# Performance work log

Hardware: AMD Instinct MI355X
Metric: run time of the kernel (lower is better)

Reference implementation:

```python
import jax, jax.numpy as jnp
import numpy as np

NUM_SCALES = 3
LAMBDA_0 = 1.0
MU_0 = 1.0
KAPPA_LAMBDA = 0.5
KAPPA_MU = 0.5
BASE_WEIGHT = 1.0
GRADIENT_SCALING = 0.1


def tgradient(f, axis):
    """torch.gradient semantics: central diff interior, one-sided at edges (spacing=1)."""
    n = f.shape[axis]
    def sl(a, b):
        idx = [slice(None)] * f.ndim
        idx[axis] = slice(a, b)
        return f[tuple(idx)]
    interior = (sl(2, n) - sl(0, n - 2)) * 0.5
    first = sl(1, 2) - sl(0, 1)
    last = sl(n - 1, n) - sl(n - 2, n - 1)
    return jnp.concatenate([first, interior, last], axis=axis)


def resize1d_linear(x, axis, out_size):
    """1D linear resize along `axis` with align_corners=True."""
    in_size = x.shape[axis]
    if out_size == in_size:
        return x
    denom = max(out_size - 1, 1)
    coords = jnp.arange(out_size, dtype=jnp.float32) * ((in_size - 1) / denom)
    i0 = jnp.floor(coords).astype(jnp.int32)
    i1 = jnp.minimum(i0 + 1, in_size - 1)
    w = (coords - i0.astype(jnp.float32)).astype(x.dtype)
    shape = [1] * x.ndim
    shape[axis] = out_size
    w = w.reshape(shape)
    x0 = jnp.take(x, i0, axis=axis)
    x1 = jnp.take(x, i1, axis=axis)
    return x0 * (1 - w) + x1 * w


def trilinear_downsample(x, scale):
    # F.interpolate(..., scale_factor=1/scale, mode='trilinear', align_corners=True,
    # recompute_scale_factor=True): out_size = floor(in_size / scale); separable linear.
    for axis in (2, 3, 4):
        out_size = int(np.floor(x.shape[axis] / scale))
        x = resize1d_linear(x, axis, out_size)
    return x


def elasticity_loss(deformation_field, image):
    total_loss = jnp.float32(0.0)
    for i in range(NUM_SCALES):
        scale = 2 ** i
        deform = trilinear_downsample(deformation_field, scale)
        img = trilinear_downsample(image, scale)
        u, v, w = deform[:, 0], deform[:, 1], deform[:, 2]  # each (B, X, Y, Z)
        du_dx, du_dy, du_dz = tgradient(u, 1), tgradient(u, 2), tgradient(u, 3)
        dv_dx, dv_dy, dv_dz = tgradient(v, 1), tgradient(v, 2), tgradient(v, 3)
        dw_dx, dw_dy, dw_dz = tgradient(w, 1), tgradient(w, 2), tgradient(w, 3)
        E_xx, E_yy, E_zz = du_dx, dv_dy, dw_dz
        E_xy = 0.5 * (du_dy + dv_dx)
        E_xz = 0.5 * (du_dz + dw_dx)
        E_yz = 0.5 * (dv_dz + dw_dy)
        trace_E = E_xx + E_yy + E_zz
        ic = img[:, 0]  # (B, X, Y, Z)
        gx, gy, gz = tgradient(ic, 1), tgradient(ic, 2), tgradient(ic, 3)
        image_gradient = jnp.sqrt(gx * gx + gy * gy + gz * gz)
        adaptive_lambda = LAMBDA_0 + KAPPA_LAMBDA * image_gradient
        adaptive_mu = MU_0 + KAPPA_MU * image_gradient
        elastic_energy = (0.5 * adaptive_lambda * trace_E ** 2
                          + adaptive_mu * (E_xx ** 2 + E_yy ** 2 + E_zz ** 2
                                           + 2.0 * (E_xy ** 2 + E_xz ** 2 + E_yz ** 2)))
        adaptive_weight = BASE_WEIGHT + GRADIENT_SCALING * image_gradient
        total_loss = total_loss + jnp.mean(adaptive_weight * elastic_energy)
    return total_loss


def setup_inputs() -> dict:
    key = jax.random.key(0)
    k1, k2 = jax.random.split(key)
    deformation_field = jax.random.normal(k1, (2, 3, 160, 192, 160), dtype=jnp.float32)
    image = jax.random.uniform(k2, (2, 1, 160, 192, 160), dtype=jnp.float32)
    return {"deformation_field": deformation_field, "image": image}


def reference(deformation_field, image):
    return elasticity_loss(deformation_field, image)
```

## Files before the change

### kernel.cpp

```cpp
#include <hip/hip_runtime.h>
#include <math.h>


#define LAMBDA_0 1.0f
#define MU_0 1.0f
#define KAPPA_LAMBDA 0.5f
#define KAPPA_MU 0.5f
#define BASE_WEIGHT 1.0f
#define GRADIENT_SCALING 0.1f

constexpr int TY = 32;
constexpr int TZ = 32;
constexpr int CX = 10;
constexpr int PITCH = TZ + 4;
constexpr int ROWS = TY + 2;
constexpr int FSZ = ROWS * PITCH;

struct P4 {
    float4 a, b, c, d;
    float ha, hb, hc, hd;
};

__device__ __forceinline__ P4 loadPlane(const float* __restrict__ p0,
                                        const float* __restrict__ p1,
                                        const float* __restrict__ p2,
                                        const float* __restrict__ p3,
                                        long long po, long long ctrOff,
                                        bool hasHalo, long long haloOff) {
    P4 r;
    long long o = po + ctrOff;
    r.a = *(const float4*)(p0 + o);
    r.b = *(const float4*)(p1 + o);
    r.c = *(const float4*)(p2 + o);
    r.d = *(const float4*)(p3 + o);
    r.ha = r.hb = r.hc = r.hd = 0.f;
    if (hasHalo) {
        long long h = po + haloOff;
        r.ha = p0[h]; r.hb = p1[h]; r.hc = p2[h]; r.hd = p3[h];
    }
    return r;
}

__device__ __forceinline__ void storePlane(float* lds, const P4& pr,
                                           int ldsCtr, bool hasHalo, int hIdx) {
    *(float4*)(lds + 0 * FSZ + ldsCtr) = pr.a;
    *(float4*)(lds + 1 * FSZ + ldsCtr) = pr.b;
    *(float4*)(lds + 2 * FSZ + ldsCtr) = pr.c;
    *(float4*)(lds + 3 * FSZ + ldsCtr) = pr.d;
    if (hasHalo) {
        lds[0 * FSZ + hIdx] = pr.ha;
        lds[1 * FSZ + hIdx] = pr.hb;
        lds[2 * FSZ + hIdx] = pr.hc;
        lds[3 * FSZ + hIdx] = pr.hd;
    }
}

__device__ __forceinline__ void unpackC(const P4& p, float d[4][4]) {
    d[0][0] = p.a.x; d[0][1] = p.a.y; d[0][2] = p.a.z; d[0][3] = p.a.w;
    d[1][0] = p.b.x; d[1][1] = p.b.y; d[1][2] = p.b.z; d[1][3] = p.b.w;
    d[2][0] = p.c.x; d[2][1] = p.c.y; d[2][2] = p.c.z; d[2][3] = p.c.w;
    d[3][0] = p.d.x; d[3][1] = p.d.y; d[3][2] = p.d.z; d[3][3] = p.d.w;
}

__global__ void elasticity_stream_kernel(const float* __restrict__ def,
                                         const float* __restrict__ img,
                                         int X, int Y, int Z,
                                         int nby, int nbz, int nbx,
                                         float inv_n, float* __restrict__ out) {
    __shared__ __align__(16) float lds[4 * FSZ];

    int t = blockIdx.x;
    const int bx = t % nbx; t /= nbx;
    const int bz = t % nbz; t /= nbz;
    const int by = t % nby; t /= nby;
    const int b = t;

    const int tz = bz * TZ, ty = by * TY, x0 = bx * CX;
    const int tid = threadIdx.x;
    const int zg = tid & 7;
    const int ly = tid >> 3;

    const long long vol = (long long)X * Y * Z;
    const long long sX = (long long)Y * Z;
    const float* __restrict__ p0 = def + ((long long)b * 3 + 0) * vol;
    const float* __restrict__ p1 = def + ((long long)b * 3 + 1) * vol;
    const float* __restrict__ p2 = def + ((long long)b * 3 + 2) * vol;
    const float* __restrict__ p3 = img + (long long)b * vol;

    const int gy = ty + ly;
    const int gz0 = tz + 4 * zg;
    const long long ctrOff = (long long)gy * Z + gz0;
    const int ldsCtr = (ly + 1) * PITCH + 4 * zg;

    const bool hasHalo = (tid < 2 * (TZ + 2) + 2 * TY);
    int hIdx = 0;
    long long haloOff = 0;
    if (hasHalo) {
        int hr, hc;
        if (tid < TZ + 2)                { hr = 0;      hc = tid; }
        else if (tid < 2 * (TZ + 2))     { hr = TY + 1; hc = tid - (TZ + 2); }
        else if (tid < 2 * (TZ + 2) + TY){ hr = tid - 2 * (TZ + 2) + 1; hc = TZ; }
        else                             { hr = tid - (2 * (TZ + 2) + TY) + 1; hc = TZ + 1; }
        int zl = (hc < TZ) ? hc : ((hc == TZ) ? -1 : TZ);
        int hy = min(max(ty + hr - 1, 0), Y - 1);
        int hz = min(max(tz + zl, 0), Z - 1);
        haloOff = (long long)hy * Z + hz;
        hIdx = hr * PITCH + hc;
    }

    const bool ylo = (gy == 0), yhi = (gy == Y - 1);
    const bool zloE = (gz0 == 0), zhiE = (gz0 + 4 == Z);
    const int zmCol = (zg == 0) ? TZ : (4 * zg - 1);
    const int zpCol = (zg == 7) ? (TZ + 1) : (4 * zg + 4);
    const int rowM = ly * PITCH + 4 * zg;
    const int rowC = (ly + 1) * PITCH;
    const int rowP = (ly + 2) * PITCH + 4 * zg;

    float Cprev[4][4], Ccur[4][4], Cnext[4][4];
    {
        long long o = (long long)max(x0 - 1, 0) * sX + ctrOff;
        float4 a = *(const float4*)(p0 + o);
        float4 bq = *(const float4*)(p1 + o);
        float4 c = *(const float4*)(p2 + o);
        float4 d = *(const float4*)(p3 + o);
        Cprev[0][0]=a.x; Cprev[0][1]=a.y; Cprev[0][2]=a.z; Cprev[0][3]=a.w;
        Cprev[1][0]=bq.x;Cprev[1][1]=bq.y;Cprev[1][2]=bq.z;Cprev[1][3]=bq.w;
        Cprev[2][0]=c.x; Cprev[2][1]=c.y; Cprev[2][2]=c.z; Cprev[2][3]=c.w;
        Cprev[3][0]=d.x; Cprev[3][1]=d.y; Cprev[3][2]=d.z; Cprev[3][3]=d.w;
    }
    P4 cur = loadPlane(p0, p1, p2, p3, (long long)x0 * sX, ctrOff, hasHalo, haloOff);
    storePlane(lds, cur, ldsCtr, hasHalo, hIdx);
    unpackC(cur, Ccur);
    __syncthreads();
    P4 pn = loadPlane(p0, p1, p2, p3, (long long)(x0 + 1) * sX, ctrOff, hasHalo, haloOff);

    float acc = 0.f;
    for (int i = 0; i < CX; ++i) {
        const int x = x0 + i;
        const bool xlo = (x == 0), xhi = (x == X - 1);

        P4 q;
        const bool more = (i + 1 < CX);
        if (more) {
            long long xp = min(x + 2, X - 1);
            q = loadPlane(p0, p1, p2, p3, xp * sX, ctrOff, hasHalo, haloOff);
        }

        unpackC(pn, Cnext);

        float GX[4][4], GY[4][4], GZ[4][4];
#pragma unroll
        for (int f = 0; f < 4; ++f) {
            const float* L = lds + f * FSZ;
            float4 ym = *(const float4*)(L + rowM);
            float4 yp = *(const float4*)(L + rowP);
            float zm = L[rowC + zmCol];
            float zp = L[rowC + zpCol];
            float ymv[4] = {ym.x, ym.y, ym.z, ym.w};
            float ypv[4] = {yp.x, yp.y, yp.z, yp.w};
#pragma unroll
            for (int i2 = 0; i2 < 4; ++i2) {
                float C = Ccur[f][i2];
                GX[f][i2] = xlo ? (Cnext[f][i2] - C)
                                : (xhi ? (C - Cprev[f][i2])
                                       : 0.5f * (Cnext[f][i2] - Cprev[f][i2]));
                GY[f][i2] = ylo ? (ypv[i2] - C)
                                : (yhi ? (C - ymv[i2])
                                       : 0.5f * (ypv[i2] - ymv[i2]));
            }
            GZ[f][0] = zloE ? (Ccur[f][1] - Ccur[f][0]) : 0.5f * (Ccur[f][1] - zm);
            GZ[f][1] = 0.5f * (Ccur[f][2] - Ccur[f][0]);
            GZ[f][2] = 0.5f * (Ccur[f][3] - Ccur[f][1]);
            GZ[f][3] = zhiE ? (Ccur[f][3] - Ccur[f][2]) : 0.5f * (zp - Ccur[f][2]);
        }

#pragma unroll
        for (int i2 = 0; i2 < 4; ++i2) {
            float Exx = GX[0][i2], Eyy = GY[1][i2], Ezz = GZ[2][i2];
            float Exy = 0.5f * (GY[0][i2] + GX[1][i2]);
            float Exz = 0.5f * (GZ[0][i2] + GX[2][i2]);
            float Eyz = 0.5f * (GZ[1][i2] + GY[2][i2]);
            float tr = Exx + Eyy + Ezz;
            float g = sqrtf(GX[3][i2] * GX[3][i2] + GY[3][i2] * GY[3][i2] +
                            GZ[3][i2] * GZ[3][i2]);
            float lam = LAMBDA_0 + KAPPA_LAMBDA * g;
            float mu  = MU_0 + KAPPA_MU * g;
            float energy = 0.5f * lam * tr * tr +
                           mu * (Exx * Exx + Eyy * Eyy + Ezz * Ezz +
                                 2.0f * (Exy * Exy + Exz * Exz + Eyz * Eyz));
            float wgt = BASE_WEIGHT + GRADIENT_SCALING * g;
            acc += wgt * energy;
        }

        if (more) {
            __syncthreads();
            storePlane(lds, pn, ldsCtr, hasHalo, hIdx);
            __syncthreads();
#pragma unroll
            for (int f = 0; f < 4; ++f)
#pragma unroll
                for (int i2 = 0; i2 < 4; ++i2) {
                    Cprev[f][i2] = Ccur[f][i2];
                    Ccur[f][i2] = Cnext[f][i2];
                }
            pn = q;
        }
    }

    float val = acc * inv_n;
    for (int off = 32; off > 0; off >>= 1)
        val += __shfl_down(val, off, 64);
    __shared__ float smem[4];
    int lane = threadIdx.x & 63;
    int wid = (int)(threadIdx.x >> 6);
    if (lane == 0) smem[wid] = val;
    __syncthreads();
    if (threadIdx.x == 0) {
        float s = smem[0] + smem[1] + smem[2] + smem[3];
        atomicAdd(out, s);
    }
}


__global__ void downsample3d_kernel(const float* __restrict__ in,
                                    float* __restrict__ out,
                                    int nmaps,
                                    int inX, int inY, int inZ,
                                    int outX, int outY, int outZ,
                                    float rx, float ry, float rz) {
    long long total = (long long)nmaps * outX * outY * outZ;
    long long idx = (long long)blockIdx.x * blockDim.x + threadIdx.x;
    if (idx >= total) return;

    int z = (int)(idx % outZ);
    long long t = idx / outZ;
    int y = (int)(t % outY);
    t /= outY;
    int x = (int)(t % outX);
    int m = (int)(t / outX);

    float cx = (float)x * rx;
    float cy = (float)y * ry;
    float cz = (float)z * rz;
    int ix0 = (int)floorf(cx), iy0 = (int)floorf(cy), iz0 = (int)floorf(cz);
    float wx = cx - (float)ix0, wy = cy - (float)iy0, wz = cz - (float)iz0;
    int ix1 = min(ix0 + 1, inX - 1);
    int iy1 = min(iy0 + 1, inY - 1);
    int iz1 = min(iz0 + 1, inZ - 1);

    long long sYZ = (long long)inY * inZ;
    const float* p = in + (long long)m * inX * sYZ;

    long long bx0 = (long long)ix0 * sYZ, bx1 = (long long)ix1 * sYZ;
    long long by0 = (long long)iy0 * inZ, by1 = (long long)iy1 * inZ;

    float v000 = p[bx0 + by0 + iz0], v001 = p[bx0 + by0 + iz1];
    float v010 = p[bx0 + by1 + iz0], v011 = p[bx0 + by1 + iz1];
    float v100 = p[bx1 + by0 + iz0], v101 = p[bx1 + by0 + iz1];
    float v110 = p[bx1 + by1 + iz0], v111 = p[bx1 + by1 + iz1];

    float a00 = v000 * (1.f - wx) + v100 * wx;
    float a01 = v001 * (1.f - wx) + v101 * wx;
    float a10 = v010 * (1.f - wx) + v110 * wx;
    float a11 = v011 * (1.f - wx) + v111 * wx;
    float b0 = a00 * (1.f - wy) + a10 * wy;
    float b1 = a01 * (1.f - wy) + a11 * wy;
    out[idx] = b0 * (1.f - wz) + b1 * wz;
}

__global__ void elasticity_loss_v4_kernel(const float* __restrict__ def,
                                          const float* __restrict__ img,
                                          int B, int X, int Y, int Z,
                                          float inv_n,
                                          float* __restrict__ out) {
    const int Zg = Z >> 2;
    long long total = (long long)B * X * Y * Zg;
    long long idx = (long long)blockIdx.x * blockDim.x + threadIdx.x;
    float val = 0.f;
    if (idx < total) {
        int zg = (int)(idx % Zg);
        long long t = idx / Zg;
        int y = (int)(t % Y);
        t /= Y;
        int x = (int)(t % X);
        int b = (int)(t / X);
        int z0 = zg << 2;

        long long vol = (long long)X * Y * Z;
        const float* base0 = def + ((long long)b * 3 + 0) * vol;
        const float* base1 = def + ((long long)b * 3 + 1) * vol;
        const float* base2 = def + ((long long)b * 3 + 2) * vol;
        const float* base3 = img + (long long)b * vol;
        const float* bases[4] = {base0, base1, base2, base3};

        long long sX = (long long)Y * Z;
        long long c = (long long)x * sX + (long long)y * Z + z0;
        long long cxm = (x > 0) ? c - sX : c;
        long long cxp = (x < X - 1) ? c + sX : c;
        long long cym = (y > 0) ? c - Z : c;
        long long cyp = (y < Y - 1) ? c + Z : c;
        long long czm = (z0 > 0) ? c - 1 : c;
        long long czp = (z0 + 4 < Z) ? c + 4 : c;

        float C[4][4], XM[4][4], XP[4][4], YM[4][4], YP[4][4];
        float ZM[4], ZP[4];
#pragma unroll
        for (int f = 0; f < 4; ++f) {
            const float* p = bases[f];
            float4 tc = *(const float4*)(p + c);
            float4 txm = *(const float4*)(p + cxm);
            float4 txp = *(const float4*)(p + cxp);
            float4 tym = *(const float4*)(p + cym);
            float4 typ = *(const float4*)(p + cyp);
            ZM[f] = p[czm];
            ZP[f] = p[czp];
            C[f][0] = tc.x;  C[f][1] = tc.y;  C[f][2] = tc.z;  C[f][3] = tc.w;
            XM[f][0] = txm.x; XM[f][1] = txm.y; XM[f][2] = txm.z; XM[f][3] = txm.w;
            XP[f][0] = txp.x; XP[f][1] = txp.y; XP[f][2] = txp.z; XP[f][3] = txp.w;
            YM[f][0] = tym.x; YM[f][1] = tym.y; YM[f][2] = tym.z; YM[f][3] = tym.w;
            YP[f][0] = typ.x; YP[f][1] = typ.y; YP[f][2] = typ.z; YP[f][3] = typ.w;
        }

        const bool xlo = (x == 0), xhi = (x == X - 1);
        const bool ylo = (y == 0), yhi = (y == Y - 1);
        const bool zlo = (z0 == 0), zhi = (z0 + 4 == Z);

        float GX[4][4], GY[4][4], GZ[4][4];
#pragma unroll
        for (int f = 0; f < 4; ++f) {
#pragma unroll
            for (int i = 0; i < 4; ++i) {
                GX[f][i] = xlo ? (XP[f][i] - C[f][i])
                               : (xhi ? (C[f][i] - XM[f][i])
                                      : 0.5f * (XP[f][i] - XM[f][i]));
                GY[f][i] = ylo ? (YP[f][i] - C[f][i])
                               : (yhi ? (C[f][i] - YM[f][i])
                                      : 0.5f * (YP[f][i] - YM[f][i]));
            }
            GZ[f][0] = zlo ? (C[f][1] - C[f][0]) : 0.5f * (C[f][1] - ZM[f]);
            GZ[f][1] = 0.5f * (C[f][2] - C[f][0]);
            GZ[f][2] = 0.5f * (C[f][3] - C[f][1]);
            GZ[f][3] = zhi ? (C[f][3] - C[f][2]) : 0.5f * (ZP[f] - C[f][2]);
        }

        float acc = 0.f;
#pragma unroll
        for (int i = 0; i < 4; ++i) {
            float Exx = GX[0][i], Eyy = GY[1][i], Ezz = GZ[2][i];
            float Exy = 0.5f * (GY[0][i] + GX[1][i]);
            float Exz = 0.5f * (GZ[0][i] + GX[2][i]);
            float Eyz = 0.5f * (GZ[1][i] + GY[2][i]);
            float tr = Exx + Eyy + Ezz;
            float g = sqrtf(GX[3][i] * GX[3][i] + GY[3][i] * GY[3][i] +
                            GZ[3][i] * GZ[3][i]);
            float lam = LAMBDA_0 + KAPPA_LAMBDA * g;
            float mu  = MU_0 + KAPPA_MU * g;
            float energy = 0.5f * lam * tr * tr +
                           mu * (Exx * Exx + Eyy * Eyy + Ezz * Ezz +
                                 2.0f * (Exy * Exy + Exz * Exz + Eyz * Eyz));
            float wgt = BASE_WEIGHT + GRADIENT_SCALING * g;
            acc += wgt * energy;
        }
        val = acc * inv_n;
    }

    for (int off = 32; off > 0; off >>= 1)
        val += __shfl_down(val, off, 64);
    __shared__ float smem[8];
    int lane = threadIdx.x & 63;
    int wid = (int)(threadIdx.x >> 6);
    if (lane == 0) smem[wid] = val;
    __syncthreads();
    if (threadIdx.x == 0) {
        float s = 0.f;
        int nw = (int)(blockDim.x >> 6);
        for (int i = 0; i < nw; ++i) s += smem[i];
        atomicAdd(out, s);
    }
}

static void launch_loss_v4(const float* def, const float* img, int B, int X,
                           int Y, int Z, float* out, hipStream_t stream) {
    const int BLOCK = 256;
    long long nvox = (long long)B * X * Y * Z;
    long long total = nvox >> 2;
    float inv_n = (float)(1.0 / (double)nvox);
    int grid = (int)((total + BLOCK - 1) / BLOCK);
    elasticity_loss_v4_kernel<<<grid, BLOCK, 0, stream>>>(def, img, B, X, Y, Z,
                                                          inv_n, out);
}

extern "C" void kernel_launch(void* const* d_in, const int* in_sizes, int n_in,
                              void* d_out, int out_size, void* d_ws, size_t ws_size,
                              hipStream_t stream) {
    const float* def = (const float*)d_in[0];
    const float* img = (const float*)d_in[1];
    float* out = (float*)d_out;

    const int B = 2;
    const int X0 = 160, Y0 = 192, Z0 = 160;

    hipMemsetAsync(out, 0, sizeof(float), stream);

    const int BLOCK = 256;

    {
        long long nvox = (long long)B * X0 * Y0 * Z0;
        float inv_n = (float)(1.0 / (double)nvox);
        int nby = Y0 / TY;
        int nbz = Z0 / TZ;
        int nbx = X0 / CX;
        int grid = B * nby * nbz * nbx;
        elasticity_stream_kernel<<<grid, 256, 0, stream>>>(def, img, X0, Y0, Z0,
                                                           nby, nbz, nbx,
                                                           inv_n, out);
    }

    const int X2 = 80, Y2 = 96, Z2 = 80;
    const int X4 = 40, Y4 = 48, Z4 = 40;
    long long vol2 = (long long)X2 * Y2 * Z2;
    long long vol4 = (long long)X4 * Y4 * Z4;

    float* def2 = (float*)d_ws;
    float* img2 = def2 + (long long)B * 3 * vol2;
    float* def4 = img2 + (long long)B * vol2;
    float* img4 = def4 + (long long)B * 3 * vol4;

    {
        float rx = (float)((double)(X0 - 1) / (double)(X2 - 1));
        float ry = (float)((double)(Y0 - 1) / (double)(Y2 - 1));
        float rz = (float)((double)(Z0 - 1) / (double)(Z2 - 1));
        long long td = (long long)B * 3 * vol2;
        int gd = (int)((td + BLOCK - 1) / BLOCK);
        downsample3d_kernel<<<gd, BLOCK, 0, stream>>>(def, def2, B * 3,
                                                      X0, Y0, Z0, X2, Y2, Z2,
                                                      rx, ry, rz);
        long long ti = (long long)B * vol2;
        int gi = (int)((ti + BLOCK - 1) / BLOCK);
        downsample3d_kernel<<<gi, BLOCK, 0, stream>>>(img, img2, B,
                                                      X0, Y0, Z0, X2, Y2, Z2,
                                                      rx, ry, rz);
        launch_loss_v4(def2, img2, B, X2, Y2, Z2, out, stream);
    }

    {
        float rx = (float)((double)(X0 - 1) / (double)(X4 - 1));
        float ry = (float)((double)(Y0 - 1) / (double)(Y4 - 1));
        float rz = (float)((double)(Z0 - 1) / (double)(Z4 - 1));
        long long td = (long long)B * 3 * vol4;
        int gd = (int)((td + BLOCK - 1) / BLOCK);
        downsample3d_kernel<<<gd, BLOCK, 0, stream>>>(def, def4, B * 3,
                                                      X0, Y0, Z0, X4, Y4, Z4,
                                                      rx, ry, rz);
        long long ti = (long long)B * vol4;
        int gi = (int)((ti + BLOCK - 1) / BLOCK);
        downsample3d_kernel<<<gi, BLOCK, 0, stream>>>(img, img4, B,
                                                      X0, Y0, Z0, X4, Y4, Z4,
                                                      rx, ry, rz);
        launch_loss_v4(def4, img4, B, X4, Y4, Z4, out, stream);
    }
}
```

Before: 116.7 us.

## Merge downsample launches, vectorize z outputs, shuffle z-neighbors, halve x-chunk

Merges the deformation and image downsample launches into one kernel per scale, where each thread computes four consecutive z outputs and writes them as a float4. In the full-resolution stream kernel, interior z-neighbor values now come from wavefront shuffles instead of LDS reads. The x-chunk per block drops from 10 to 5, giving more blocks but more halo plane reloads. The merged kernel hardcodes 8 maps (B=2), which fits the test shape but is less general.

```diff
diff --git a/kernel.cpp b/kernel.cpp
--- a/kernel.cpp
+++ b/kernel.cpp
@@ -11,7 +11,7 @@
 
 constexpr int TY = 32;
 constexpr int TZ = 32;
-constexpr int CX = 10;
+constexpr int CX = 5;
 constexpr int PITCH = TZ + 4;
 constexpr int ROWS = TY + 2;
 constexpr int FSZ = ROWS * PITCH;
@@ -79,6 +79,9 @@
     const int tid = threadIdx.x;
     const int zg = tid & 7;
     const int ly = tid >> 3;
+    const int lane = tid & 63;
+    const int laneM = (lane - 1) & 63;
+    const int laneP = (lane + 1) & 63;
 
     const long long vol = (long long)X * Y * Z;
     const long long sX = (long long)Y * Z;
@@ -110,8 +113,6 @@
 
     const bool ylo = (gy == 0), yhi = (gy == Y - 1);
     const bool zloE = (gz0 == 0), zhiE = (gz0 + 4 == Z);
-    const int zmCol = (zg == 0) ? TZ : (4 * zg - 1);
-    const int zpCol = (zg == 7) ? (TZ + 1) : (4 * zg + 4);
     const int rowM = ly * PITCH + 4 * zg;
     const int rowC = (ly + 1) * PITCH;
     const int rowP = (ly + 2) * PITCH + 4 * zg;
@@ -154,8 +155,10 @@
             const float* L = lds + f * FSZ;
             float4 ym = *(const float4*)(L + rowM);
             float4 yp = *(const float4*)(L + rowP);
-            float zm = L[rowC + zmCol];
-            float zp = L[rowC + zpCol];
+            float zmv = __shfl(Ccur[f][3], laneM, 64);
+            float zpv = __shfl(Ccur[f][0], laneP, 64);
+            float zm = (zg == 0) ? L[rowC + TZ] : zmv;
+            float zp = (zg == 7) ? L[rowC + TZ + 1] : zpv;
             float ymv[4] = {ym.x, ym.y, ym.z, ym.w};
             float ypv[4] = {yp.x, yp.y, yp.z, yp.w};
 #pragma unroll
@@ -211,9 +214,8 @@
     for (int off = 32; off > 0; off >>= 1)
         val += __shfl_down(val, off, 64);
     __shared__ float smem[4];
-    int lane = threadIdx.x & 63;
     int wid = (int)(threadIdx.x >> 6);
-    if (lane == 0) smem[wid] = val;
+    if ((threadIdx.x & 63) == 0) smem[wid] = val;
     __syncthreads();
     if (threadIdx.x == 0) {
         float s = smem[0] + smem[1] + smem[2] + smem[3];
@@ -221,51 +223,73 @@
     }
 }
 
-
-__global__ void downsample3d_kernel(const float* __restrict__ in,
-                                    float* __restrict__ out,
-                                    int nmaps,
-                                    int inX, int inY, int inZ,
-                                    int outX, int outY, int outZ,
-                                    float rx, float ry, float rz) {
-    long long total = (long long)nmaps * outX * outY * outZ;
+__global__ void downsample_all_kernel(const float* __restrict__ def,
+                                      const float* __restrict__ img,
+                                      float* __restrict__ odef,
+                                      float* __restrict__ oimg,
+                                      int inX, int inY, int inZ,
+                                      int outX, int outY, int outZ,
+                                      float rx, float ry, float rz) {
+    const int NDEF = 6;
+    const int NMAP = 8;
+    const int outZ4 = outZ >> 2;
+    long long total = (long long)NMAP * outX * outY * outZ4;
     long long idx = (long long)blockIdx.x * blockDim.x + threadIdx.x;
     if (idx >= total) return;
 
-    int z = (int)(idx % outZ);
-    long long t = idx / outZ;
+    int zq = (int)(idx % outZ4);
+    long long t = idx / outZ4;
     int y = (int)(t % outY);
     t /= outY;
     int x = (int)(t % outX);
     int m = (int)(t / outX);
 
+    long long invol = (long long)inX * inY * inZ;
+    long long outvol = (long long)outX * outY * outZ;
+    const float* src;
+    float* dst;
+    if (m < NDEF) { src = def + (long long)m * invol; dst = odef + (long long)m * outvol; }
+    else          { src = img + (long long)(m - NDEF) * invol; dst = oimg + (long long)(m - NDEF) * outvol; }
+
     float cx = (float)x * rx;
     float cy = (float)y * ry;
-    float cz = (float)z * rz;
-    int ix0 = (int)floorf(cx), iy0 = (int)floorf(cy), iz0 = (int)floorf(cz);
-    float wx = cx - (float)ix0, wy = cy - (float)iy0, wz = cz - (float)iz0;
+    int ix0 = (int)floorf(cx), iy0 = (int)floorf(cy);
+    float wx = cx - (float)ix0, wy = cy - (float)iy0;
     int ix1 = min(ix0 + 1, inX - 1);
     int iy1 = min(iy0 + 1, inY - 1);
-    int iz1 = min(iz0 + 1, inZ - 1);
 
     long long sYZ = (long long)inY * inZ;
-    const float* p = in + (long long)m * inX * sYZ;
-
     long long bx0 = (long long)ix0 * sYZ, bx1 = (long long)ix1 * sYZ;
     long long by0 = (long long)iy0 * inZ, by1 = (long long)iy1 * inZ;
-
-    float v000 = p[bx0 + by0 + iz0], v001 = p[bx0 + by0 + iz1];
-    float v010 = p[bx0 + by1 + iz0], v011 = p[bx0 + by1 + iz1];
-    float v100 = p[bx1 + by0 + iz0], v101 = p[bx1 + by0 + iz1];
-    float v110 = p[bx1 + by1 + iz0], v111 = p[bx1 + by1 + iz1];
-
-    float a00 = v000 * (1.f - wx) + v100 * wx;
-    float a01 = v001 * (1.f - wx) + v101 * wx;
-    float a10 = v010 * (1.f - wx) + v110 * wx;
-    float a11 = v011 * (1.f - wx) + v111 * wx;
-    float b0 = a00 * (1.f - wy) + a10 * wy;
-    float b1 = a01 * (1.f - wy) + a11 * wy;
-    out[idx] = b0 * (1.f - wz) + b1 * wz;
+    const float* r00 = src + bx0 + by0;
+    const float* r01 = src + bx0 + by1;
+    const float* r10 = src + bx1 + by0;
+    const float* r11 = src + bx1 + by1;
+
+    int z0 = zq << 2;
+    float res[4];
+#pragma unroll
+    for (int j = 0; j < 4; ++j) {
+        float cz = (float)(z0 + j) * rz;
+        int iz0 = (int)floorf(cz);
+        float wz = cz - (float)iz0;
+        int iz1 = min(iz0 + 1, inZ - 1);
+
+        float v000 = r00[iz0], v001 = r00[iz1];
+        float v010 = r01[iz0], v011 = r01[iz1];
+        float v100 = r10[iz0], v101 = r10[iz1];
+        float v110 = r11[iz0], v111 = r11[iz1];
+
+        float a00 = v000 * (1.f - wx) + v100 * wx;
+        float a01 = v001 * (1.f - wx) + v101 * wx;
+        float a10 = v010 * (1.f - wx) + v110 * wx;
+        float a11 = v011 * (1.f - wx) + v111 * wx;
+        float b0 = a00 * (1.f - wy) + a10 * wy;
+        float b1 = a01 * (1.f - wy) + a11 * wy;
+        res[j] = b0 * (1.f - wz) + b1 * wz;
+    }
+    *(float4*)(dst + ((long long)x * outY + y) * outZ + z0) =
+        make_float4(res[0], res[1], res[2], res[3]);
 }
 
 __global__ void elasticity_loss_v4_kernel(const float* __restrict__ def,
@@ -430,16 +454,11 @@
         float rx = (float)((double)(X0 - 1) / (double)(X2 - 1));
         float ry = (float)((double)(Y0 - 1) / (double)(Y2 - 1));
         float rz = (float)((double)(Z0 - 1) / (double)(Z2 - 1));
-        long long td = (long long)B * 3 * vol2;
-        int gd = (int)((td + BLOCK - 1) / BLOCK);
-        downsample3d_kernel<<<gd, BLOCK, 0, stream>>>(def, def2, B * 3,
-                                                      X0, Y0, Z0, X2, Y2, Z2,
-                                                      rx, ry, rz);
-        long long ti = (long long)B * vol2;
-        int gi = (int)((ti + BLOCK - 1) / BLOCK);
-        downsample3d_kernel<<<gi, BLOCK, 0, stream>>>(img, img2, B,
-                                                      X0, Y0, Z0, X2, Y2, Z2,
-                                                      rx, ry, rz);
+        long long total = 8LL * X2 * Y2 * (Z2 >> 2);
+        int g = (int)((total + BLOCK - 1) / BLOCK);
+        downsample_all_kernel<<<g, BLOCK, 0, stream>>>(def, img, def2, img2,
+                                                       X0, Y0, Z0, X2, Y2, Z2,
+                                                       rx, ry, rz);
         launch_loss_v4(def2, img2, B, X2, Y2, Z2, out, stream);
     }
 
@@ -447,16 +466,11 @@
         float rx = (float)((double)(X0 - 1) / (double)(X4 - 1));
         float ry = (float)((double)(Y0 - 1) / (double)(Y4 - 1));
         float rz = (float)((double)(Z0 - 1) / (double)(Z4 - 1));
-        long long td = (long long)B * 3 * vol4;
-        int gd = (int)((td + BLOCK - 1) / BLOCK);
-        downsample3d_kernel<<<gd, BLOCK, 0, stream>>>(def, def4, B * 3,
-                                                      X0, Y0, Z0, X4, Y4, Z4,
-                                                      rx, ry, rz);
-        long long ti = (long long)B * vol4;
-        int gi = (int)((ti + BLOCK - 1) / BLOCK);
-        downsample3d_kernel<<<gi, BLOCK, 0, stream>>>(img, img4, B,
-                                                      X0, Y0, Z0, X4, Y4, Z4,
-                                                      rx, ry, rz);
+        long long total = 8LL * X4 * Y4 * (Z4 >> 2);
+        int g = (int)((total + BLOCK - 1) / BLOCK);
+        downsample_all_kernel<<<g, BLOCK, 0, stream>>>(def, img, def4, img4,
+                                                       X0, Y0, Z0, X4, Y4, Z4,
+                                                       rx, ry, rz);
         launch_loss_v4(def4, img4, B, X4, Y4, Z4, out, stream);
     }
 }
```

Result: slower. 173.8 us (+49.0%).
